# Performance work log

Hardware: AMD Instinct MI355X
Metric: run time of the kernel (lower is better)

## Reference

```python
import jax, jax.numpy as jnp
import numpy as np

N_NODES = 50000
N_EDGES = 1_600_000
Q_MULT = 8          # charges_irreps = 8x0e
NODE_MULT = 64      # node_feat_irreps = 64x0e + 64x1o
RBF = 8             # edge_feats_irreps num_irreps
HID = 64            # FullyConnectedNet hidden width
W_NUMEL = 2 * Q_MULT  # edge_tp weight_numel: two uvu paths (0e->0e, 0e x 1o->1o), u=8


def setup_inputs() -> dict:
    key = jax.random.key(0)
    k = jax.random.split(key, 14)
    f = lambda kk, sh: jax.random.normal(kk, sh, dtype=jnp.float32)
    return {
        "node_feats": f(k[0], (N_NODES, NODE_MULT * 4)),          # 64 scalars + 64 vectors(3)
        "charges_0": f(k[1], (N_NODES, Q_MULT)),                  # unused in forward
        "charges_induced": f(k[2], (N_NODES, Q_MULT)),
        "edge_feats": f(k[3], (N_EDGES, RBF)),
        "edge_attrs": f(k[4], (N_EDGES, 4)),                      # Y0 (1) + Y1 (3)
        "field_feats": f(k[5], (N_NODES, RBF)),                   # unused in forward
        "mlp_w1": f(k[6], (RBF, HID)),
        "mlp_w2": f(k[7], (HID, HID)),
        "mlp_w3": f(k[8], (HID, HID)),
        "mlp_w4": f(k[9], (HID, W_NUMEL)),
        "W0": f(k[10], (Q_MULT, NODE_MULT)),                      # node_tp path 0e x 0e -> 0e
        "W1": f(k[11], (Q_MULT, NODE_MULT)),                      # node_tp path 1o x 1o -> 0e
        "edge_index": jax.random.randint(k[12], (2, N_EDGES), 0, N_NODES, dtype=jnp.int32),
        "batch": jnp.zeros((N_NODES,), dtype=jnp.int32),
    }


def reference(node_feats, charges_0, charges_induced, edge_feats, edge_attrs,
              field_feats, mlp_w1, mlp_w2, mlp_w3, mlp_w4, W0, W1,
              edge_index, batch):
    sender, receiver = edge_index[0], edge_index[1]
    num_nodes = node_feats.shape[0]

    # e3nn FullyConnectedNet: variance-normalized linear layers + silu
    h = edge_feats
    for w in (mlp_w1, mlp_w2, mlp_w3):
        h = jax.nn.silu(h @ (w / np.sqrt(np.float32(w.shape[0]))))
    tp_w = h @ (mlp_w4 / np.sqrt(np.float32(mlp_w4.shape[0])))   # [E, 16]
    w0, w1 = tp_w[:, :Q_MULT], tp_w[:, Q_MULT:]                   # per-edge path weights

    # edge_tp (uvu, external weights): gather sender charges, weighted CG product
    q_s = charges_induced[sender]                                  # [E, 8]
    mid0 = (w0 * q_s) * edge_attrs[:, :1]                          # [E, 8]    0e
    mid1 = (w1 * q_s)[:, :, None] * edge_attrs[:, None, 1:4]       # [E, 8, 3] 1o

    # scatter-sum messages to receiver nodes
    sum0 = jax.ops.segment_sum(mid0, receiver, num_segments=num_nodes)
    sum1 = jax.ops.segment_sum(mid1.reshape(-1, Q_MULT * 3), receiver,
                               num_segments=num_nodes).reshape(-1, Q_MULT, 3)

    # node_tp: FullyConnectedTensorProduct(8x0e+8x1o, 64x0e+64x1o -> 1x0e)
    node0 = node_feats[:, :NODE_MULT]                              # [N, 64]
    node1 = node_feats[:, NODE_MULT:].reshape(-1, NODE_MULT, 3)    # [N, 64, 3]
    c = 1.0 / np.sqrt(np.float32(Q_MULT * NODE_MULT * 2))          # path normalization
    e0 = jnp.einsum('nu,nv,uv->n', sum0, node0, W0)
    e1 = jnp.einsum('nuk,nvk,uv->n', sum1, node1, W1) / np.sqrt(np.float32(3.0))  # w3j(1,1,0)
    return c * (e0 + e1)                                           # [N] per-node energy
```

## Files before the change

### kernel.cpp

```cpp
#include <hip/hip_runtime.h>
#include <hip/hip_bf16.h>

typedef short short8 __attribute__((ext_vector_type(8)));
typedef float f32x4 __attribute__((ext_vector_type(4)));

static __device__ __forceinline__ float bf2f(unsigned int b) { return __uint_as_float(b << 16); }
static __device__ __forceinline__ short fb2s(float x) {
    unsigned u = __float_as_uint(x);
    return (short)((u + 0x7FFFu + ((u >> 16) & 1u)) >> 16);
}
static __device__ __forceinline__ unsigned int pack2(float lo, float hi) {
    unsigned int r;
    asm("v_cvt_pk_bf16_f32 %0, %1, %2" : "=v"(r) : "v"(lo), "v"(hi));
    return r;
}
static __device__ __forceinline__ float silu(float x) {
    return x * __builtin_amdgcn_rcpf(1.0f + __expf(-x));
}
static __device__ __forceinline__ float load1(const void* p, long off, int isbf) {
    return isbf ? bf2f(((const unsigned short*)p)[off]) : ((const float*)p)[off];
}
static __device__ __forceinline__ void load4(const void* p, long off, int isbf, float* o) {
    if (isbf) {
        uint2 v = *(const uint2*)((const unsigned short*)p + off);
        o[0]=bf2f(v.x&0xffffu); o[1]=bf2f(v.x>>16);
        o[2]=bf2f(v.y&0xffffu); o[3]=bf2f(v.y>>16);
    } else {
        float4 v = *(const float4*)((const float*)p + off);
        o[0]=v.x; o[1]=v.y; o[2]=v.z; o[3]=v.w;
    }
}
static __device__ __forceinline__ int detect_bf16(const void* nf) {
    const unsigned int* w = (const unsigned int*)nf;
    int lane = threadIdx.x & 63;
    unsigned int e = (w[lane] >> 7) & 0xFFu;
    unsigned long long m = __ballot(e >= 118u && e <= 132u);
    return __popcll(m) >= 32 ? 1 : 0;
}

#define NB 32
__global__ __launch_bounds__(256) void k_node(
    const void* __restrict__ nf, const void* __restrict__ W0, const void* __restrict__ W1,
    const void* __restrict__ w1, const void* __restrict__ w2,
    const void* __restrict__ w3, const void* __restrict__ w4,
    short* __restrict__ Bws, float* __restrict__ NA, float* __restrict__ acc, int n_nodes) {
    __shared__ float Nd0[NB * 68];
    __shared__ float Nd1[3 * NB * 68];
    __shared__ float W0L[8 * 68];
    __shared__ float W1L[8 * 68];
    const int tid = threadIdx.x;
    const int isbf = detect_bf16(nf);
    const long n0 = (long)blockIdx.x * NB;

    if (blockIdx.x < 44) {
        int idx = blockIdx.x * 256 + tid;
        int j = idx & 7, lane = (idx >> 3) & 63, tile = idx >> 9;
        int n16 = lane & 15, kq = lane >> 4;
        float v;
        if (tile < 4) {
            int k = kq * 8 + j, n = tile * 16 + n16;
            v = (k < 8) ? load1(w1, k * 64 + n, isbf) * 0.35355339059327373f : 0.0f;
        } else if (tile < 12) {
            int t = (tile - 4) >> 1, kt = (tile - 4) & 1;
            int k = kt * 32 + kq * 8 + j, n = t * 16 + n16;
            v = load1(w2, k * 64 + n, isbf) * 0.125f;
        } else if (tile < 20) {
            int t = (tile - 12) >> 1, kt = (tile - 12) & 1;
            int k = kt * 32 + kq * 8 + j, n = t * 16 + n16;
            v = load1(w3, k * 64 + n, isbf) * 0.125f;
        } else {
            int kt = tile - 20;
            int k = kt * 32 + kq * 8 + j, n = n16;
            v = load1(w4, k * 16 + n, isbf) * 0.125f;
        }
        Bws[idx] = fb2s(v);
    }
    if (tid < NB) {
        long n = n0 + tid;
        if (n < n_nodes) acc[n] = 0.0f;
    }
    if (n0 >= n_nodes) return;

    for (int i = tid; i < 512; i += 256) {
        W0L[(i >> 6) * 68 + (i & 63)] = load1(W0, i, isbf);
        W1L[(i >> 6) * 68 + (i & 63)] = load1(W1, i, isbf);
    }
    if (isbf) {
        for (int i = tid; i < NB * 32; i += 256) {
            int node = i >> 5, c8 = (i & 31) * 8;
            long ng = n0 + node; if (ng > n_nodes - 1) ng = n_nodes - 1;
            uint4 v = *(const uint4*)((const unsigned short*)nf + ng * 256 + c8);
            float f[8];
            f[0]=bf2f(v.x&0xffffu); f[1]=bf2f(v.x>>16);
            f[2]=bf2f(v.y&0xffffu); f[3]=bf2f(v.y>>16);
            f[4]=bf2f(v.z&0xffffu); f[5]=bf2f(v.z>>16);
            f[6]=bf2f(v.w&0xffffu); f[7]=bf2f(v.w>>16);
            #pragma unroll
            for (int t = 0; t < 8; t++) {
                int col = c8 + t;
                if (col < 64) Nd0[node * 68 + col] = f[t];
                else {
                    int cc = col - 64, vv = cc / 3, kk = cc - vv * 3;
                    Nd1[(kk * NB + node) * 68 + vv] = f[t];
                }
            }
        }
    } else {
        for (int i = tid; i < NB * 64; i += 256) {
            int node = i >> 6, c4 = (i & 63) * 4;
            long ng = n0 + node; if (ng > n_nodes - 1) ng = n_nodes - 1;
            float4 v = *(const float4*)((const float*)nf + ng * 256 + c4);
            float f[4] = {v.x, v.y, v.z, v.w};
            #pragma unroll
            for (int t = 0; t < 4; t++) {
                int col = c4 + t;
                if (col < 64) Nd0[node * 68 + col] = f[t];
                else {
                    int cc = col - 64, vv = cc / 3, kk = cc - vv * 3;
                    Nd1[(kk * NB + node) * 68 + vv] = f[t];
                }
            }
        }
    }
    __syncthreads();

    const int wv = tid >> 6, lane = tid & 63;
    const int u = lane & 7, ln = lane >> 3;
    float sum[4] = {0.0f, 0.0f, 0.0f, 0.0f};

    if (wv == 0) {
        const float* w = &W0L[u * 68];
        for (int v0 = 0; v0 < 64; v0 += 4) {
            float4 w4 = *(const float4*)(w + v0);
            #pragma unroll
            for (int j = 0; j < 4; j++) {
                float4 nd = *(const float4*)&Nd0[(ln + 8 * j) * 68 + v0];
                sum[j] += w4.x * nd.x + w4.y * nd.y + w4.z * nd.z + w4.w * nd.w;
            }
        }
        #pragma unroll
        for (int j = 0; j < 4; j++) {
            long node = n0 + ln + 8 * j;
            if (node < n_nodes) NA[node * 32 + u] = sum[j] * 0.03125f;
        }
    } else {
        const int kk = wv - 1;
        const float* w = &W1L[u * 68];
        const float* nd1 = &Nd1[kk * NB * 68];
        for (int v0 = 0; v0 < 64; v0 += 4) {
            float4 w4 = *(const float4*)(w + v0);
            #pragma unroll
            for (int j = 0; j < 4; j++) {
                float4 nd = *(const float4*)&nd1[(ln + 8 * j) * 68 + v0];
                sum[j] += w4.x * nd.x + w4.y * nd.y + w4.z * nd.z + w4.w * nd.w;
            }
        }
        #pragma unroll
        for (int j = 0; j < 4; j++) {
            long node = n0 + ln + 8 * j;
            if (node < n_nodes) NA[node * 32 + 8 + u * 3 + kk] = sum[j] * 0.018042195912175804f;
        }
    }
}

__global__ __launch_bounds__(256, 4) void k_edges_mfma(
    const void* __restrict__ ef, const void* __restrict__ ea, const void* __restrict__ qc,
    const int* __restrict__ eidx, const void* __restrict__ nf,
    const short* __restrict__ Bws, const float* __restrict__ NA,
    float* __restrict__ acc, int n_edges) {
    __shared__ __align__(16) short W[11264];
    __shared__ __align__(16) short Hs[4 * 2304];
    const int tid = threadIdx.x, lane = tid & 63, wv = tid >> 6;
    const int n16 = lane & 15, kq = lane >> 4;
    const int isbf = detect_bf16(nf);

    {
        const uint4* src = (const uint4*)Bws;
        uint4* dst = (uint4*)W;
        for (int i = tid; i < 1408; i += 256) dst[i] = src[i];
    }
    __syncthreads();

    short* Hw = Hs + wv * 2304;
    const int rbit = (n16 >> 3) & 1;
    const int wrow = n16 * 72 + ((kq & 1) << 2);
    const f32x4 zero = {0.0f, 0.0f, 0.0f, 0.0f};

    for (int half = 0; half < 2; half++) {
        const long E0 = (long)blockIdx.x * 256 + half * 128 + wv * 32;

        const int el = lane >> 1, h = lane & 1;
        const long e_ep = E0 + el;
        long ec = e_ep; if (ec > n_edges - 1) ec = n_edges - 1;
        const int s_nd = eidx[ec];
        const int r_nd = eidx[(long)n_edges + ec];
        float eav[4];
        load4(ea, ec * 4, isbf, eav);

        short8 a1[2];
        #pragma unroll
        for (int nt = 0; nt < 2; nt++) {
            short8 a = {0,0,0,0,0,0,0,0};
            if (kq == 0) {
                long e = E0 + nt * 16 + n16;
                if (e > n_edges - 1) e = n_edges - 1;
                if (isbf) {
                    a = *(const short8*)((const unsigned short*)ef + e * 8);
                } else {
                    const float* pe = (const float*)ef + e * 8;
                    float4 v0 = *(const float4*)pe, v1 = *(const float4*)(pe + 4);
                    a[0]=fb2s(v0.x); a[1]=fb2s(v0.y); a[2]=fb2s(v0.z); a[3]=fb2s(v0.w);
                    a[4]=fb2s(v1.x); a[5]=fb2s(v1.y); a[6]=fb2s(v1.z); a[7]=fb2s(v1.w);
                }
            }
            a1[nt] = a;
        }

        {
            f32x4 c1[2][4];
            #pragma unroll
            for (int t = 0; t < 4; t++) {
                short8 b = *(const short8*)(W + t * 512 + lane * 8);
                #pragma unroll
                for (int nt = 0; nt < 2; nt++)
                    c1[nt][t] = __builtin_amdgcn_mfma_f32_16x16x32_bf16(b, a1[nt], zero, 0, 0, 0);
            }
            #pragma unroll
            for (int nt = 0; nt < 2; nt++)
                #pragma unroll
                for (int t = 0; t < 4; t++) {
                    uint2 pkd;
                    pkd.x = pack2(silu(c1[nt][t][0]), silu(c1[nt][t][1]));
                    pkd.y = pack2(silu(c1[nt][t][2]), silu(c1[nt][t][3]));
                    *(uint2*)(Hw + nt * 1152 + wrow + (((t * 2 + (kq >> 1)) ^ rbit) << 3)) = pkd;
                }
        }

        float q[4];
        load4(qc, (long)s_nd * 8 + h * 4, isbf, q);
        const float* nr = NA + (long)r_nd * 32;
        float4 n0 = *(const float4*)(nr + h * 4);
        float t12[12];
        *(float4*)(t12 + 0) = *(const float4*)(nr + 8 + h * 12);
        *(float4*)(t12 + 4) = *(const float4*)(nr + 12 + h * 12);
        *(float4*)(t12 + 8) = *(const float4*)(nr + 16 + h * 12);

        #pragma unroll
        for (int L = 0; L < 2; L++) {
            const int base = (L == 0) ? 4 : 12;
            short8 aH[2][2];
            #pragma unroll
            for (int nt = 0; nt < 2; nt++)
                #pragma unroll
                for (int kt = 0; kt < 2; kt++)
                    aH[nt][kt] = *(const short8*)(Hw + nt * 1152 + n16 * 72 + (((kt * 4 + kq) ^ rbit) << 3));
            f32x4 c2[2][4];
            #pragma unroll
            for (int nt = 0; nt < 2; nt++)
                #pragma unroll
                for (int t = 0; t < 4; t++) c2[nt][t] = zero;
            #pragma unroll
            for (int kt = 0; kt < 2; kt++)
                #pragma unroll
                for (int t = 0; t < 4; t++) {
                    short8 b = *(const short8*)(W + (base + t * 2 + kt) * 512 + lane * 8);
                    #pragma unroll
                    for (int nt = 0; nt < 2; nt++)
                        c2[nt][t] = __builtin_amdgcn_mfma_f32_16x16x32_bf16(b, aH[nt][kt], c2[nt][t], 0, 0, 0);
                }
            #pragma unroll
            for (int nt = 0; nt < 2; nt++)
                #pragma unroll
                for (int t = 0; t < 4; t++) {
                    uint2 pkd;
                    pkd.x = pack2(silu(c2[nt][t][0]), silu(c2[nt][t][1]));
                    pkd.y = pack2(silu(c2[nt][t][2]), silu(c2[nt][t][3]));
                    *(uint2*)(Hw + nt * 1152 + wrow + (((t * 2 + (kq >> 1)) ^ rbit) << 3)) = pkd;
                }
        }

        float* TP = (float*)Hw;
        {
            short8 aH[2][2];
            #pragma unroll
            for (int nt = 0; nt < 2; nt++)
                #pragma unroll
                for (int kt = 0; kt < 2; kt++)
                    aH[nt][kt] = *(const short8*)(Hw + nt * 1152 + n16 * 72 + (((kt * 4 + kq) ^ rbit) << 3));
            f32x4 c4[2] = {zero, zero};
            #pragma unroll
            for (int kt = 0; kt < 2; kt++) {
                short8 b = *(const short8*)(W + (20 + kt) * 512 + lane * 8);
                #pragma unroll
                for (int nt = 0; nt < 2; nt++)
                    c4[nt] = __builtin_amdgcn_mfma_f32_16x16x32_bf16(b, aH[nt][kt], c4[nt], 0, 0, 0);
            }
            #pragma unroll
            for (int nt = 0; nt < 2; nt++)
                *(f32x4*)(TP + (nt * 16 + n16) * 20 + (kq << 2)) = c4[nt];
        }

        {
            float4 t0 = *(const float4*)(TP + el * 20 + h * 4);
            float4 t1 = *(const float4*)(TP + el * 20 + 8 + h * 4);
            float tp0[4] = {t0.x, t0.y, t0.z, t0.w};
            float tp1[4] = {t1.x, t1.y, t1.z, t1.w};
            float n0a[4] = {n0.x, n0.y, n0.z, n0.w};
            float p = 0.0f;
            #pragma unroll
            for (int i = 0; i < 4; i++) {
                float d = eav[1] * t12[i * 3] + eav[2] * t12[i * 3 + 1] + eav[3] * t12[i * 3 + 2];
                p += tp0[i] * q[i] * eav[0] * n0a[i] + tp1[i] * q[i] * d;
            }
            p += __shfl_xor(p, 1);
            if (h == 0 && e_ep < n_edges) atomicAdd(&acc[r_nd], p);
        }
    }
}

__global__ void k_out(const float* __restrict__ acc, void* __restrict__ out,
                      const void* __restrict__ nf, int n) {
    const int isbf = detect_bf16(nf);
    int i = blockIdx.x * 256 + threadIdx.x;
    if (i >= n) return;
    if (isbf) ((__hip_bfloat16*)out)[i] = __float2bfloat16(acc[i]);
    else      ((float*)out)[i] = acc[i];
}

extern "C" void kernel_launch(void* const* d_in, const int* in_sizes, int n_in,
                              void* d_out, int out_size, void* d_ws, size_t ws_size,
                              hipStream_t stream) {
    const void* node_feats      = d_in[0];
    const void* charges_induced = d_in[2];
    const void* edge_feats      = d_in[3];
    const void* edge_attrs      = d_in[4];
    const void* mlp_w1          = d_in[6];
    const void* mlp_w2          = d_in[7];
    const void* mlp_w3          = d_in[8];
    const void* mlp_w4          = d_in[9];
    const void* W0              = d_in[10];
    const void* W1              = d_in[11];
    const int*  edge_index      = (const int*)d_in[12];

    const int n_nodes = in_sizes[0] / 256;
    const int n_edges = in_sizes[3] / 8;

    short* Bws = (short*)d_ws;
    float* NA  = (float*)((char*)d_ws + 22528);
    float* acc = NA + (size_t)n_nodes * 32;

    int nblk = (n_nodes + NB - 1) / NB;
    if (nblk < 44) nblk = 44;
    k_node<<<nblk, 256, 0, stream>>>(node_feats, W0, W1,
        mlp_w1, mlp_w2, mlp_w3, mlp_w4, Bws, NA, acc, n_nodes);
    k_edges_mfma<<<(n_edges + 255) / 256, 256, 0, stream>>>(
        edge_feats, edge_attrs, charges_induced, edge_index, node_feats, Bws, NA, acc, n_edges);
    k_out<<<(n_nodes + 255) / 256, 256, 0, stream>>>(acc, d_out, node_feats, n_nodes);
}
```

Before: 317.9 us.

## Process one 16-edge tile per pass, fold exp scaling into weights, raise occupancy

```diff
diff --git a/kernel.cpp b/kernel.cpp
--- a/kernel.cpp
+++ b/kernel.cpp
@@ -14,8 +14,8 @@
     asm("v_cvt_pk_bf16_f32 %0, %1, %2" : "=v"(r) : "v"(lo), "v"(hi));
     return r;
 }
-static __device__ __forceinline__ float silu(float x) {
-    return x * __builtin_amdgcn_rcpf(1.0f + __expf(-x));
+static __device__ __forceinline__ float hsilu(float y) {
+    return y * __builtin_amdgcn_rcpf(1.0f + __builtin_amdgcn_exp2f(-y));
 }
 static __device__ __forceinline__ float load1(const void* p, long off, int isbf) {
     return isbf ? bf2f(((const unsigned short*)p)[off]) : ((const float*)p)[off];
@@ -59,7 +59,7 @@
         float v;
         if (tile < 4) {
             int k = kq * 8 + j, n = tile * 16 + n16;
-            v = (k < 8) ? load1(w1, k * 64 + n, isbf) * 0.35355339059327373f : 0.0f;
+            v = (k < 8) ? load1(w1, k * 64 + n, isbf) * (0.35355339059327373f * 1.4426950408889634f) : 0.0f;
         } else if (tile < 12) {
             int t = (tile - 4) >> 1, kt = (tile - 4) & 1;
             int k = kt * 32 + kq * 8 + j, n = t * 16 + n16;
@@ -71,7 +71,7 @@
         } else {
             int kt = tile - 20;
             int k = kt * 32 + kq * 8 + j, n = n16;
-            v = load1(w4, k * 16 + n, isbf) * 0.125f;
+            v = load1(w4, k * 16 + n, isbf) * (0.125f * 0.6931471805599453f);
         }
         Bws[idx] = fb2s(v);
     }
@@ -163,13 +163,13 @@
     }
 }
 
-__global__ __launch_bounds__(256, 4) void k_edges_mfma(
+__global__ __launch_bounds__(256, 5) void k_edges_mfma(
     const void* __restrict__ ef, const void* __restrict__ ea, const void* __restrict__ qc,
     const int* __restrict__ eidx, const void* __restrict__ nf,
     const short* __restrict__ Bws, const float* __restrict__ NA,
     float* __restrict__ acc, int n_edges) {
     __shared__ __align__(16) short W[11264];
-    __shared__ __align__(16) short Hs[4 * 2304];
+    __shared__ __align__(16) short Hs[4 * 1152];
     const int tid = threadIdx.x, lane = tid & 63, wv = tid >> 6;
     const int n16 = lane & 15, kq = lane >> 4;
     const int isbf = detect_bf16(nf);
@@ -181,139 +181,120 @@
     }
     __syncthreads();
 
-    short* Hw = Hs + wv * 2304;
+    short* Hw = Hs + wv * 1152;
     const int rbit = (n16 >> 3) & 1;
     const int wrow = n16 * 72 + ((kq & 1) << 2);
+    const int kql = (kq & 1) << 2;
     const f32x4 zero = {0.0f, 0.0f, 0.0f, 0.0f};
 
     for (int half = 0; half < 2; half++) {
-        const long E0 = (long)blockIdx.x * 256 + half * 128 + wv * 32;
-
-        const int el = lane >> 1, h = lane & 1;
-        const long e_ep = E0 + el;
-        long ec = e_ep; if (ec > n_edges - 1) ec = n_edges - 1;
-        const int s_nd = eidx[ec];
-        const int r_nd = eidx[(long)n_edges + ec];
-        float eav[4];
-        load4(ea, ec * 4, isbf, eav);
-
-        short8 a1[2];
         #pragma unroll
         for (int nt = 0; nt < 2; nt++) {
-            short8 a = {0,0,0,0,0,0,0,0};
+            const long E0 = (long)blockIdx.x * 256 + half * 128 + wv * 32 + nt * 16;
+            const long e = E0 + n16;
+            long ec = e; if (ec > n_edges - 1) ec = n_edges - 1;
+
+            const int s_nd = eidx[ec];
+            const int r_nd = eidx[(long)n_edges + ec];
+            float eav[4];
+            load4(ea, ec * 4, isbf, eav);
+
+            short8 a1 = {0,0,0,0,0,0,0,0};
             if (kq == 0) {
-                long e = E0 + nt * 16 + n16;
-                if (e > n_edges - 1) e = n_edges - 1;
                 if (isbf) {
-                    a = *(const short8*)((const unsigned short*)ef + e * 8);
+                    a1 = *(const short8*)((const unsigned short*)ef + ec * 8);
                 } else {
-                    const float* pe = (const float*)ef + e * 8;
+                    const float* pe = (const float*)ef + ec * 8;
                     float4 v0 = *(const float4*)pe, v1 = *(const float4*)(pe + 4);
-                    a[0]=fb2s(v0.x); a[1]=fb2s(v0.y); a[2]=fb2s(v0.z); a[3]=fb2s(v0.w);
-                    a[4]=fb2s(v1.x); a[5]=fb2s(v1.y); a[6]=fb2s(v1.z); a[7]=fb2s(v1.w);
-                }
-            }
-            a1[nt] = a;
-        }
-
-        {
-            f32x4 c1[2][4];
-            #pragma unroll
-            for (int t = 0; t < 4; t++) {
-                short8 b = *(const short8*)(W + t * 512 + lane * 8);
-                #pragma unroll
-                for (int nt = 0; nt < 2; nt++)
-                    c1[nt][t] = __builtin_amdgcn_mfma_f32_16x16x32_bf16(b, a1[nt], zero, 0, 0, 0);
-            }
-            #pragma unroll
-            for (int nt = 0; nt < 2; nt++)
+                    a1[0]=fb2s(v0.x); a1[1]=fb2s(v0.y); a1[2]=fb2s(v0.z); a1[3]=fb2s(v0.w);
+                    a1[4]=fb2s(v1.x); a1[5]=fb2s(v1.y); a1[6]=fb2s(v1.z); a1[7]=fb2s(v1.w);
+                }
+            }
+
+            {
+                f32x4 c1[4];
+                #pragma unroll
+                for (int t = 0; t < 4; t++) {
+                    short8 b = *(const short8*)(W + t * 512 + lane * 8);
+                    c1[t] = __builtin_amdgcn_mfma_f32_16x16x32_bf16(b, a1, zero, 0, 0, 0);
+                }
                 #pragma unroll
                 for (int t = 0; t < 4; t++) {
                     uint2 pkd;
-                    pkd.x = pack2(silu(c1[nt][t][0]), silu(c1[nt][t][1]));
-                    pkd.y = pack2(silu(c1[nt][t][2]), silu(c1[nt][t][3]));
-                    *(uint2*)(Hw + nt * 1152 + wrow + (((t * 2 + (kq >> 1)) ^ rbit) << 3)) = pkd;
-                }
-        }
-
-        float q[4];
-        load4(qc, (long)s_nd * 8 + h * 4, isbf, q);
-        const float* nr = NA + (long)r_nd * 32;
-        float4 n0 = *(const float4*)(nr + h * 4);
-        float t12[12];
-        *(float4*)(t12 + 0) = *(const float4*)(nr + 8 + h * 12);
-        *(float4*)(t12 + 4) = *(const float4*)(nr + 12 + h * 12);
-        *(float4*)(t12 + 8) = *(const float4*)(nr + 16 + h * 12);
-
-        #pragma unroll
-        for (int L = 0; L < 2; L++) {
-            const int base = (L == 0) ? 4 : 12;
-            short8 aH[2][2];
-            #pragma unroll
-            for (int nt = 0; nt < 2; nt++)
+                    pkd.x = pack2(hsilu(c1[t][0]), hsilu(c1[t][1]));
+                    pkd.y = pack2(hsilu(c1[t][2]), hsilu(c1[t][3]));
+                    *(uint2*)(Hw + wrow + (((t * 2 + (kq >> 1)) ^ rbit) << 3)) = pkd;
+                }
+            }
+
+            float q4[4];
+            load4(qc, (long)s_nd * 8 + kql, isbf, q4);
+            float na[12];
+            const float* nr = NA + (long)r_nd * 32;
+            if (kq < 2) {
+                *(float4*)na = *(const float4*)(nr + (kq << 2));
+            } else {
+                *(float4*)(na + 0) = *(const float4*)(nr + 8 + (kq - 2) * 12);
+                *(float4*)(na + 4) = *(const float4*)(nr + 12 + (kq - 2) * 12);
+                *(float4*)(na + 8) = *(const float4*)(nr + 16 + (kq - 2) * 12);
+            }
+
+            #pragma unroll
+            for (int L = 0; L < 2; L++) {
+                const int base = (L == 0) ? 4 : 12;
+                short8 aH[2];
                 #pragma unroll
                 for (int kt = 0; kt < 2; kt++)
-                    aH[nt][kt] = *(const short8*)(Hw + nt * 1152 + n16 * 72 + (((kt * 4 + kq) ^ rbit) << 3));
-            f32x4 c2[2][4];
-            #pragma unroll
-            for (int nt = 0; nt < 2; nt++)
-                #pragma unroll
-                for (int t = 0; t < 4; t++) c2[nt][t] = zero;
-            #pragma unroll
-            for (int kt = 0; kt < 2; kt++)
-                #pragma unroll
-                for (int t = 0; t < 4; t++) {
-                    short8 b = *(const short8*)(W + (base + t * 2 + kt) * 512 + lane * 8);
+                    aH[kt] = *(const short8*)(Hw + n16 * 72 + (((kt * 4 + kq) ^ rbit) << 3));
+                f32x4 c2[4];
+                #pragma unroll
+                for (int t = 0; t < 4; t++) c2[t] = zero;
+                #pragma unroll
+                for (int kt = 0; kt < 2; kt++)
                     #pragma unroll
-                    for (int nt = 0; nt < 2; nt++)
-                        c2[nt][t] = __builtin_amdgcn_mfma_f32_16x16x32_bf16(b, aH[nt][kt], c2[nt][t], 0, 0, 0);
-                }
-            #pragma unroll
-            for (int nt = 0; nt < 2; nt++)
+                    for (int t = 0; t < 4; t++) {
+                        short8 b = *(const short8*)(W + (base + t * 2 + kt) * 512 + lane * 8);
+                        c2[t] = __builtin_amdgcn_mfma_f32_16x16x32_bf16(b, aH[kt], c2[t], 0, 0, 0);
+                    }
                 #pragma unroll
                 for (int t = 0; t < 4; t++) {
                     uint2 pkd;
-                    pkd.x = pack2(silu(c2[nt][t][0]), silu(c2[nt][t][1]));
-                    pkd.y = pack2(silu(c2[nt][t][2]), silu(c2[nt][t][3]));
-                    *(uint2*)(Hw + nt * 1152 + wrow + (((t * 2 + (kq >> 1)) ^ rbit) << 3)) = pkd;
-                }
-        }
-
-        float* TP = (float*)Hw;
-        {
-            short8 aH[2][2];
-            #pragma unroll
-            for (int nt = 0; nt < 2; nt++)
+                    pkd.x = pack2(hsilu(c2[t][0]), hsilu(c2[t][1]));
+                    pkd.y = pack2(hsilu(c2[t][2]), hsilu(c2[t][3]));
+                    *(uint2*)(Hw + wrow + (((t * 2 + (kq >> 1)) ^ rbit) << 3)) = pkd;
+                }
+            }
+
+            f32x4 c4 = zero;
+            {
+                short8 aH[2];
                 #pragma unroll
                 for (int kt = 0; kt < 2; kt++)
-                    aH[nt][kt] = *(const short8*)(Hw + nt * 1152 + n16 * 72 + (((kt * 4 + kq) ^ rbit) << 3));
-            f32x4 c4[2] = {zero, zero};
-            #pragma unroll
-            for (int kt = 0; kt < 2; kt++) {
-                short8 b = *(const short8*)(W + (20 + kt) * 512 + lane * 8);
-                #pragma unroll
-                for (int nt = 0; nt < 2; nt++)
-                    c4[nt] = __builtin_amdgcn_mfma_f32_16x16x32_bf16(b, aH[nt][kt], c4[nt], 0, 0, 0);
-            }
-            #pragma unroll
-            for (int nt = 0; nt < 2; nt++)
-                *(f32x4*)(TP + (nt * 16 + n16) * 20 + (kq << 2)) = c4[nt];
-        }
-
-        {
-            float4 t0 = *(const float4*)(TP + el * 20 + h * 4);
-            float4 t1 = *(const float4*)(TP + el * 20 + 8 + h * 4);
-            float tp0[4] = {t0.x, t0.y, t0.z, t0.w};
-            float tp1[4] = {t1.x, t1.y, t1.z, t1.w};
-            float n0a[4] = {n0.x, n0.y, n0.z, n0.w};
-            float p = 0.0f;
-            #pragma unroll
-            for (int i = 0; i < 4; i++) {
-                float d = eav[1] * t12[i * 3] + eav[2] * t12[i * 3 + 1] + eav[3] * t12[i * 3 + 2];
-                p += tp0[i] * q[i] * eav[0] * n0a[i] + tp1[i] * q[i] * d;
-            }
-            p += __shfl_xor(p, 1);
-            if (h == 0 && e_ep < n_edges) atomicAdd(&acc[r_nd], p);
+                    aH[kt] = *(const short8*)(Hw + n16 * 72 + (((kt * 4 + kq) ^ rbit) << 3));
+                #pragma unroll
+                for (int kt = 0; kt < 2; kt++) {
+                    short8 b = *(const short8*)(W + (20 + kt) * 512 + lane * 8);
+                    c4 = __builtin_amdgcn_mfma_f32_16x16x32_bf16(b, aH[kt], c4, 0, 0, 0);
+                }
+            }
+
+            {
+                float p = 0.0f;
+                if (kq < 2) {
+                    #pragma unroll
+                    for (int r = 0; r < 4; r++) p += c4[r] * q4[r] * na[r];
+                    p *= eav[0];
+                } else {
+                    #pragma unroll
+                    for (int r = 0; r < 4; r++) {
+                        float d = eav[1] * na[r * 3] + eav[2] * na[r * 3 + 1] + eav[3] * na[r * 3 + 2];
+                        p += c4[r] * q4[r] * d;
+                    }
+                }
+                p += __shfl_xor(p, 16);
+                p += __shfl_xor(p, 32);
+                if (kq == 0 && e < n_edges) atomicAdd(&acc[r_nd], p);
+            }
         }
     }
 }
```

Measured after the change: 320.4 us. Within noise of the previous version (+0.8%).
